# Performance work log

Measured on AMD Instinct MI355X. Metric: run time of the kernel, lower is better.

Reference implementation:

```python
import jax, jax.numpy as jnp
import numpy as np

EPS = 1e-5  # BatchNorm1d default eps


def gcn_conv(x, row, col, w, n):
    # symmetric normalized aggregation: out[c] = sum_e d[row]^-1/2 d[col]^-1/2 w_e x[row]
    deg = jax.ops.segment_sum(w, col, num_segments=n)           # weighted in-degree [N]
    dinv = jnp.where(deg > 0, jax.lax.rsqrt(deg), 0.0)          # nan_to_num guard
    norm = dinv[row] * dinv[col] * w                            # [E]
    msg = x[row] * norm[:, None]                                # [E, H] gather
    return jax.ops.segment_sum(msg, col, num_segments=n)        # [N, H] scatter-add


def batchnorm(x):
    # BatchNorm1d(affine=False, track_running_stats=False): batch stats, biased var
    mu = jnp.mean(x, axis=0)
    var = jnp.mean((x - mu) ** 2, axis=0)
    return (x - mu) * jax.lax.rsqrt(var + EPS)


def setup_inputs() -> dict:
    key = jax.random.key(0)
    ks = jax.random.split(key, 7)
    N, E, D, H = 100000, 1600000, 128, 128
    x = jax.random.normal(ks[0], (N, D), dtype=jnp.float32)
    edge_index = jax.random.randint(ks[1], (2, E), 0, N, dtype=jnp.int32)
    edge_weight = jax.random.uniform(ks[2], (E,), dtype=jnp.float32)
    # xavier_uniform gain=1: limit = sqrt(6/(fan_in+fan_out))
    lim0 = float(np.sqrt(6.0 / (D + H)))
    lim1 = float(np.sqrt(6.0 / (H + H)))
    W0 = jax.random.uniform(ks[3], (H, D), dtype=jnp.float32, minval=-lim0, maxval=lim0)
    W1 = jax.random.uniform(ks[4], (H, H), dtype=jnp.float32, minval=-lim1, maxval=lim1)
    b0 = jnp.zeros((H,), jnp.float32)
    b1 = jnp.zeros((H,), jnp.float32)
    return {"x": x, "edge_index": edge_index, "edge_weight": edge_weight,
            "W0": W0, "b0": b0, "W1": W1, "b1": b1}


def reference(x, edge_index, edge_weight, W0, b0, W1, b1):
    n = x.shape[0]
    row, col = edge_index[0], edge_index[1]
    # layer 0: linear -> gcn_conv -> bias -> batchnorm -> relu
    h = x @ W0.T
    h = gcn_conv(h, row, col, edge_weight, n)
    h = jax.nn.relu(batchnorm(h + b0))
    # final layer: linear -> gcn_conv -> bias
    h = h @ W1.T
    h = gcn_conv(h, row, col, edge_weight, n)
    return h + b1
```

## Files before the change

### kernel.cpp

```cpp
#include <hip/hip_runtime.h>
#include <cstdint>
#include <cstddef>

#define EPSF 1e-5f
#define BKT 256
#define BKT_SHIFT 8
#define SC_E 4096

typedef unsigned long long ull;
typedef __attribute__((ext_vector_type(8))) short bf16x8;
typedef __attribute__((ext_vector_type(4))) float f32x4;


__global__ __launch_bounds__(512) void bucket_hist(const int* __restrict__ col,
                                                   int* __restrict__ bhist, int E, int NB) {
    __shared__ int lh[512];
    const int t = threadIdx.x;
    lh[t] = 0;
    __syncthreads();
    for (int e = blockIdx.x * 512 + t; e < E; e += gridDim.x * 512)
        atomicAdd(&lh[col[e] >> BKT_SHIFT], 1);
    __syncthreads();
    if (t < NB && lh[t]) atomicAdd(&bhist[t], lh[t]);
}

__global__ __launch_bounds__(512) void scan_buckets(const int* __restrict__ bhist,
                                                    int* __restrict__ bstart,
                                                    int* __restrict__ bcursor,
                                                    int* __restrict__ rs,
                                                    int NB, int N, int E) {
    __shared__ int part[512];
    const int t = threadIdx.x;
    part[t] = (t < NB) ? bhist[t] : 0;
    __syncthreads();
    for (int off = 1; off < 512; off <<= 1) {
        int v = (t >= off) ? part[t - off] : 0;
        __syncthreads();
        part[t] += v;
        __syncthreads();
    }
    int excl = (t == 0) ? 0 : part[t - 1];
    if (t < NB) { bstart[t] = excl; bcursor[t] = excl; }
    if (t == 0) { bstart[NB] = E; rs[N] = E; }
}

__global__ __launch_bounds__(512) void bucket_scatter(const int* __restrict__ row,
                                                      const int* __restrict__ col,
                                                      const float* __restrict__ w,
                                                      int* __restrict__ bcursor,
                                                      int2* __restrict__ brecs,
                                                      int E, int NB) {
    __shared__ int lh[512], lstart[512], lcur[512], gbase[512];
    __shared__ int   sm[SC_E];
    __shared__ float sw[SC_E];
    __shared__ short sb[SC_E];

    const int t = threadIdx.x;
    const int base = blockIdx.x * SC_E;
    const int cnt = min(SC_E, E - base);

    lh[t] = 0;
    __syncthreads();

    int   myb[8], mym[8];
    float myw[8];
#pragma unroll
    for (int k = 0; k < 8; ++k) {
        int i = t + k * 512;
        if (i < cnt) {
            int e = base + i;
            int r = row[e], c = col[e];
            myb[k] = c >> BKT_SHIFT;
            mym[k] = ((c & (BKT - 1)) << 17) | r;
            myw[k] = w[e];
            atomicAdd(&lh[myb[k]], 1);
        } else myb[k] = -1;
    }
    __syncthreads();

    int v = lh[t];
    lstart[t] = v;
    __syncthreads();
    for (int off = 1; off < 512; off <<= 1) {
        int u = (t >= off) ? lstart[t - off] : 0;
        __syncthreads();
        lstart[t] += u;
        __syncthreads();
    }
    int excl = lstart[t] - v;
    __syncthreads();
    lstart[t] = excl;
    lcur[t]   = excl;
    gbase[t]  = (t < NB) ? atomicAdd(&bcursor[t], v) : 0;
    __syncthreads();

#pragma unroll
    for (int k = 0; k < 8; ++k) {
        if (myb[k] >= 0) {
            int slot = atomicAdd(&lcur[myb[k]], 1);
            sm[slot] = mym[k];
            sw[slot] = myw[k];
            sb[slot] = (short)myb[k];
        }
    }
    __syncthreads();

    for (int j = t; j < cnt; j += 512) {
        int b = sb[j];
        int pos = gbase[b] + (j - lstart[b]);
        brecs[pos] = make_int2(sm[j], __float_as_int(sw[j]));
    }
}

__global__ __launch_bounds__(256) void bucket_build(const int2* __restrict__ brecs,
                                                    const int* __restrict__ bstart,
                                                    int* __restrict__ rs,
                                                    float* __restrict__ dinv,
                                                    int2* __restrict__ sedge, int N) {
    __shared__ int   lcnt[256], lscan[256], lcur[256];
    __shared__ float ldeg[256];
    const int b = blockIdx.x, t = threadIdx.x;
    const int s = bstart[b], e = bstart[b + 1];
    const int node0 = b << BKT_SHIFT;
    const int nNodes = min(BKT, N - node0);

    lcnt[t] = 0;
    ldeg[t] = 0.f;
    __syncthreads();

    for (int i = s + t; i < e; i += 256) {
        int2 r = brecs[i];
        int cl = r.x >> 17;
        atomicAdd(&lcnt[cl], 1);
        atomicAdd(&ldeg[cl], __int_as_float(r.y));
    }
    __syncthreads();

    int v = lcnt[t];
    lscan[t] = v;
    __syncthreads();
    for (int off = 1; off < 256; off <<= 1) {
        int u = (t >= off) ? lscan[t - off] : 0;
        __syncthreads();
        lscan[t] += u;
        __syncthreads();
    }
    int excl = lscan[t] - v;
    lcur[t] = excl;
    if (t < nNodes) {
        rs[node0 + t] = s + excl;
        float d = ldeg[t];
        dinv[node0 + t] = (d > 0.f) ? rsqrtf(d) : 0.f;
    }
    __syncthreads();

    for (int i = s + t; i < e; i += 256) {
        int2 r = brecs[i];
        int slot = atomicAdd(&lcur[r.x >> 17], 1);
        sedge[s + slot] = r;
    }
}

__global__ __launch_bounds__(256) void norm_fixup(const int* __restrict__ bstart,
                                                  const float* __restrict__ dinv,
                                                  int2* __restrict__ sedge, int N) {
    __shared__ float ld[256];
    const int b = blockIdx.x, t = threadIdx.x;
    const int node0 = b << BKT_SHIFT;
    const int nNodes = min(BKT, N - node0);
    ld[t] = (t < nNodes) ? dinv[node0 + t] : 0.f;
    const int s = bstart[b], e = bstart[b + 1];
    __syncthreads();
    for (int i = s + t; i < e; i += 256) {
        int2 r = sedge[i];
        int rowi = r.x & 0x1FFFF;
        int cl = r.x >> 17;
        float nrm = dinv[rowi] * ld[cl] * __int_as_float(r.y);
        sedge[i] = make_int2(rowi, __float_as_int(nrm));
    }
}

__device__ __forceinline__ ushort f2bf(float f) {
    uint b = __float_as_uint(f);
    return (ushort)((b + 0x7FFFu + ((b >> 16) & 1u)) >> 16);
}
__device__ __forceinline__ float bf2f(ushort u) {
    return __uint_as_float((uint)u << 16);
}
__device__ __forceinline__ uint4 pack8(const float* f) {
    uint4 o;
    o.x = f2bf(f[0]) | ((uint)f2bf(f[1]) << 16);
    o.y = f2bf(f[2]) | ((uint)f2bf(f[3]) << 16);
    o.z = f2bf(f[4]) | ((uint)f2bf(f[5]) << 16);
    o.w = f2bf(f[6]) | ((uint)f2bf(f[7]) << 16);
    return o;
}

template <int MODE>
__global__ __launch_bounds__(256) void gemm128_mfma(const void* __restrict__ Xv,
                                                    const float* __restrict__ W,
                                                    ushort* __restrict__ Y, int N,
                                                    const float* __restrict__ sums,
                                                    float invN) {
    __shared__ __align__(16) ushort Alds[64][128];
    __shared__ __align__(16) ushort Blds[128][128];
    __shared__ float bnmu[128], bnrs[128];

    const int t  = threadIdx.x;
    const int n0 = blockIdx.x * 64;

    if constexpr (MODE == 2) {
        if (t < 128) {
            float mu  = sums[t] * invN;
            float var = sums[128 + t] * invN - mu * mu;
            bnmu[t] = mu;
            bnrs[t] = rsqrtf(var + EPSF);
        }
        __syncthreads();
    }

    for (int i = t; i < 128 * 16; i += 256) {
        int j = i >> 4, kc = (i & 15) << 3;
        float f[8];
        *(float4*)&f[0] = *(const float4*)&W[j * 128 + kc];
        *(float4*)&f[4] = *(const float4*)&W[j * 128 + kc + 4];
        *(uint4*)&Blds[j][kc ^ ((j & 7) << 3)] = pack8(f);
    }
    for (int i = t; i < 64 * 16; i += 256) {
        int r = i >> 4, kc = (i & 15) << 3;
        int n = n0 + r;
        uint4 v = make_uint4(0u, 0u, 0u, 0u);
        if (n < N) {
            if constexpr (MODE == 0) {
                float f[8];
                *(float4*)&f[0] = *(const float4*)&((const float*)Xv)[(size_t)n * 128 + kc];
                *(float4*)&f[4] = *(const float4*)&((const float*)Xv)[(size_t)n * 128 + kc + 4];
                v = pack8(f);
            } else {
                uint4 raw = *(const uint4*)&((const ushort*)Xv)[(size_t)n * 128 + kc];
                const uint* rw = &raw.x;
                float f[8];
#pragma unroll
                for (int k = 0; k < 4; ++k) {
                    float lo = __uint_as_float(rw[k] << 16);
                    float hi = __uint_as_float(rw[k] & 0xFFFF0000u);
                    f[2 * k]     = fmaxf((lo - bnmu[kc + 2 * k])     * bnrs[kc + 2 * k],     0.f);
                    f[2 * k + 1] = fmaxf((hi - bnmu[kc + 2 * k + 1]) * bnrs[kc + 2 * k + 1], 0.f);
                }
                v = pack8(f);
            }
        }
        *(uint4*)&Alds[r][kc ^ ((r & 7) << 3)] = v;
    }
    __syncthreads();

    const int lane  = t & 63;
    const int wv    = t >> 6;
    const int arow  = wv * 16 + (lane & 15);
    const int klane = (lane >> 4) << 3;
    const int cq    = lane & 15;

    f32x4 acc[8] = {};

    for (int ks = 0; ks < 4; ++ks) {
        const int k0 = ks * 32 + klane;
        bf16x8 a = *(const bf16x8*)&Alds[arow][k0 ^ ((arow & 7) << 3)];
#pragma unroll
        for (int tl = 0; tl < 8; ++tl) {
            int colr = tl * 16 + cq;
            bf16x8 bb = *(const bf16x8*)&Blds[colr][k0 ^ ((colr & 7) << 3)];
            acc[tl] = __builtin_amdgcn_mfma_f32_16x16x32_bf16(a, bb, acc[tl], 0, 0, 0);
        }
    }

    const int r0 = n0 + wv * 16 + ((lane >> 4) << 2);
#pragma unroll
    for (int tl = 0; tl < 8; ++tl) {
#pragma unroll
        for (int reg = 0; reg < 4; ++reg) {
            int rr = r0 + reg;
            if (rr < N) Y[(size_t)rr * 128 + tl * 16 + cq] = f2bf(acc[tl][reg]);
        }
    }
}

__device__ __forceinline__ float bflo(uint v) { return __uint_as_float(v << 16); }
__device__ __forceinline__ float bfhi(uint v) { return __uint_as_float(v & 0xFFFF0000u); }

template <bool OUT_BF16>
__global__ __launch_bounds__(256) void agg_gather(const ushort* __restrict__ Hin,
                                                  const int2* __restrict__ sedge,
                                                  const int* __restrict__ rs,
                                                  const float* __restrict__ bias,
                                                  void* __restrict__ Hout, int N, int E) {
    int c = blockIdx.x * 4 + (threadIdx.x >> 6);
    if (c >= N) return;
    const int lane = threadIdx.x & 63;

    float2 acc;
    if (bias) { acc.x = bias[lane * 2]; acc.y = bias[lane * 2 + 1]; }
    else      { acc.x = 0.f; acc.y = 0.f; }

    const int e0 = rs[c];
    const int deg = rs[c + 1] - e0;

    for (int base = 0; base < deg; base += 64) {
        int m = min(64, deg - base);
        int idx = e0 + base + lane;
        int2 rec = sedge[idx < E ? idx : E - 1];

        int j = 0;
        for (; j + 3 < m; j += 4) {
            int   r0 = __shfl(rec.x, j),     r1 = __shfl(rec.x, j + 1);
            int   r2 = __shfl(rec.x, j + 2), r3 = __shfl(rec.x, j + 3);
            float w0 = __int_as_float(__shfl(rec.y, j));
            float w1 = __int_as_float(__shfl(rec.y, j + 1));
            float w2 = __int_as_float(__shfl(rec.y, j + 2));
            float w3 = __int_as_float(__shfl(rec.y, j + 3));
            uint v0 = *(const uint*)&Hin[(size_t)r0 * 128 + lane * 2];
            uint v1 = *(const uint*)&Hin[(size_t)r1 * 128 + lane * 2];
            uint v2 = *(const uint*)&Hin[(size_t)r2 * 128 + lane * 2];
            uint v3 = *(const uint*)&Hin[(size_t)r3 * 128 + lane * 2];
            acc.x = fmaf(w0, bflo(v0), acc.x); acc.y = fmaf(w0, bfhi(v0), acc.y);
            acc.x = fmaf(w1, bflo(v1), acc.x); acc.y = fmaf(w1, bfhi(v1), acc.y);
            acc.x = fmaf(w2, bflo(v2), acc.x); acc.y = fmaf(w2, bfhi(v2), acc.y);
            acc.x = fmaf(w3, bflo(v3), acc.x); acc.y = fmaf(w3, bfhi(v3), acc.y);
        }
        for (; j < m; ++j) {
            int   r0 = __shfl(rec.x, j);
            float w0 = __int_as_float(__shfl(rec.y, j));
            uint v0 = *(const uint*)&Hin[(size_t)r0 * 128 + lane * 2];
            acc.x = fmaf(w0, bflo(v0), acc.x); acc.y = fmaf(w0, bfhi(v0), acc.y);
        }
    }

    if constexpr (OUT_BF16) {
        ((uint*)Hout)[(size_t)c * 64 + lane] = f2bf(acc.x) | ((uint)f2bf(acc.y) << 16);
    } else {
        *(float2*)&((float*)Hout)[(size_t)c * 128 + lane * 2] = acc;
    }
}

__global__ __launch_bounds__(256) void bn_stats(const ushort* __restrict__ H,
                                                float* __restrict__ sums, int N) {
    int j = threadIdx.x & 127;
    float s = 0.f, s2 = 0.f;
    for (int n = blockIdx.x * 2 + (threadIdx.x >> 7); n < N; n += gridDim.x * 2) {
        float v = bf2f(H[(size_t)n * 128 + j]);
        s += v; s2 += v * v;
    }
    atomicAdd(&sums[j], s);
    atomicAdd(&sums[128 + j], s2);
}

extern "C" void kernel_launch(void* const* d_in, const int* in_sizes, int n_in,
                              void* d_out, int out_size, void* d_ws, size_t ws_size,
                              hipStream_t stream) {
    const float* x  = (const float*)d_in[0];
    const int*   ei = (const int*)d_in[1];
    const float* ew = (const float*)d_in[2];
    const float* W0 = (const float*)d_in[3];
    const float* W1 = (const float*)d_in[5];
    const float* b1 = (const float*)d_in[6];

    const int N = in_sizes[0] / 128;
    const int E = in_sizes[2];
    const int* row = ei;
    const int* col = ei + E;
    const int NB = (N + BKT - 1) >> BKT_SHIFT;

    uintptr_t base = (uintptr_t)d_ws;
    auto alloc = [&](size_t bytes) {
        uintptr_t p = base;
        base += (bytes + 255) & ~(size_t)255;
        return (void*)p;
    };
    float*  dinv   = (float*) alloc((size_t)N * 4);
    float*  sums   = (float*) alloc(256 * 4);
    int*    bhist  = (int*)   alloc((size_t)(NB + 1) * 4);
    int*    bstart = (int*)   alloc((size_t)(NB + 1) * 4);
    int*    bcursor= (int*)   alloc((size_t)NB * 4);
    int*    rs     = (int*)   alloc((size_t)(N + 1) * 4);
    int2*   sedge  = (int2*)  alloc((size_t)E * 8);
    ushort* hA     = (ushort*)alloc((size_t)N * 128 * 2);
    ushort* hB     = (ushort*)alloc((size_t)N * 128 * 2);
    int2*   brecs  = (int2*)hB;
    float*  out    = (float*) d_out;
    (void)ws_size; (void)n_in; (void)out_size;

    const float invN = 1.f / (float)N;

    hipMemsetAsync(bhist, 0, (size_t)(NB + 1) * 4, stream);
    hipMemsetAsync(sums, 0, 256 * 4, stream);

    bucket_hist<<<1024, 512, 0, stream>>>(col, bhist, E, NB);
    scan_buckets<<<1, 512, 0, stream>>>(bhist, bstart, bcursor, rs, NB, N, E);
    bucket_scatter<<<(E + SC_E - 1) / SC_E, 512, 0, stream>>>(row, col, ew, bcursor,
                                                              brecs, E, NB);
    bucket_build<<<NB, 256, 0, stream>>>(brecs, bstart, rs, dinv, sedge, N);
    norm_fixup<<<NB, 256, 0, stream>>>(bstart, dinv, sedge, N);

    gemm128_mfma<0><<<(N + 63) / 64, 256, 0, stream>>>(x, W0, hA, N, nullptr, 0.f);

    agg_gather<true><<<(N + 3) / 4, 256, 0, stream>>>(hA, sedge, rs, nullptr, hB, N, E);

    bn_stats<<<512, 256, 0, stream>>>(hB, sums, N);

    gemm128_mfma<2><<<(N + 63) / 64, 256, 0, stream>>>(hB, W1, hA, N, sums, invN);

    agg_gather<false><<<(N + 3) / 4, 256, 0, stream>>>(hA, sedge, rs, b1, out, N, E);
}
```

Before: 305.6 us.

## Fuse norm fixup into edge placement, persist GEMM tiles, widen gather to half-wave edges

Three changes land together. The bucket build is split so that degree/dinv is computed first, and the placement pass then writes final normalized edge records directly, which removes the separate sedge re-read and re-write pass. The GEMM becomes a persistent grid-stride kernel capped at 512 blocks, so the bf16 weight tile is packed once per block instead of once per 64-row tile. The aggregation gather now has each half-wave process a different edge with 8-byte loads and combines the halves with a shuffle, raising memory-level parallelism per wave at the cost of a final reduction.

```diff
diff --git a/kernel.cpp b/kernel.cpp
--- a/kernel.cpp
+++ b/kernel.cpp
@@ -112,12 +112,11 @@
     }
 }
 
-__global__ __launch_bounds__(256) void bucket_build(const int2* __restrict__ brecs,
-                                                    const int* __restrict__ bstart,
-                                                    int* __restrict__ rs,
-                                                    float* __restrict__ dinv,
-                                                    int2* __restrict__ sedge, int N) {
-    __shared__ int   lcnt[256], lscan[256], lcur[256];
+__global__ __launch_bounds__(256) void bucket_build_p1(const int2* __restrict__ brecs,
+                                                       const int* __restrict__ bstart,
+                                                       int* __restrict__ rs,
+                                                       float* __restrict__ dinv, int N) {
+    __shared__ int   lcnt[256], lscan[256];
     __shared__ float ldeg[256];
     const int b = blockIdx.x, t = threadIdx.x;
     const int s = bstart[b], e = bstart[b + 1];
@@ -145,38 +144,36 @@
         lscan[t] += u;
         __syncthreads();
     }
-    int excl = lscan[t] - v;
-    lcur[t] = excl;
     if (t < nNodes) {
-        rs[node0 + t] = s + excl;
+        rs[node0 + t] = s + (lscan[t] - v);
         float d = ldeg[t];
         dinv[node0 + t] = (d > 0.f) ? rsqrtf(d) : 0.f;
     }
+}
+
+__global__ __launch_bounds__(256) void bucket_place(const int2* __restrict__ brecs,
+                                                    const int* __restrict__ bstart,
+                                                    const int* __restrict__ rs,
+                                                    const float* __restrict__ dinv,
+                                                    int2* __restrict__ sedge, int N) {
+    __shared__ int   lcur[256];
+    __shared__ float ld[256];
+    const int b = blockIdx.x, t = threadIdx.x;
+    const int s = bstart[b], e = bstart[b + 1];
+    const int node0 = b << BKT_SHIFT;
+    const int nNodes = min(BKT, N - node0);
+
+    lcur[t] = (t < nNodes) ? rs[node0 + t] : 0;
+    ld[t]   = (t < nNodes) ? dinv[node0 + t] : 0.f;
     __syncthreads();
 
     for (int i = s + t; i < e; i += 256) {
         int2 r = brecs[i];
-        int slot = atomicAdd(&lcur[r.x >> 17], 1);
-        sedge[s + slot] = r;
-    }
-}
-
-__global__ __launch_bounds__(256) void norm_fixup(const int* __restrict__ bstart,
-                                                  const float* __restrict__ dinv,
-                                                  int2* __restrict__ sedge, int N) {
-    __shared__ float ld[256];
-    const int b = blockIdx.x, t = threadIdx.x;
-    const int node0 = b << BKT_SHIFT;
-    const int nNodes = min(BKT, N - node0);
-    ld[t] = (t < nNodes) ? dinv[node0 + t] : 0.f;
-    const int s = bstart[b], e = bstart[b + 1];
-    __syncthreads();
-    for (int i = s + t; i < e; i += 256) {
-        int2 r = sedge[i];
+        int cl   = r.x >> 17;
         int rowi = r.x & 0x1FFFF;
-        int cl = r.x >> 17;
         float nrm = dinv[rowi] * ld[cl] * __int_as_float(r.y);
-        sedge[i] = make_int2(rowi, __float_as_int(nrm));
+        int slot = atomicAdd(&lcur[cl], 1);
+        sedge[slot] = make_int2(rowi, __float_as_int(nrm));
     }
 }
 
@@ -206,8 +203,7 @@
     __shared__ __align__(16) ushort Blds[128][128];
     __shared__ float bnmu[128], bnrs[128];
 
-    const int t  = threadIdx.x;
-    const int n0 = blockIdx.x * 64;
+    const int t = threadIdx.x;
 
     if constexpr (MODE == 2) {
         if (t < 128) {
@@ -216,7 +212,6 @@
             bnmu[t] = mu;
             bnrs[t] = rsqrtf(var + EPSF);
         }
-        __syncthreads();
     }
 
     for (int i = t; i < 128 * 16; i += 256) {
@@ -226,60 +221,66 @@
         *(float4*)&f[4] = *(const float4*)&W[j * 128 + kc + 4];
         *(uint4*)&Blds[j][kc ^ ((j & 7) << 3)] = pack8(f);
     }
-    for (int i = t; i < 64 * 16; i += 256) {
-        int r = i >> 4, kc = (i & 15) << 3;
-        int n = n0 + r;
-        uint4 v = make_uint4(0u, 0u, 0u, 0u);
-        if (n < N) {
-            if constexpr (MODE == 0) {
-                float f[8];
-                *(float4*)&f[0] = *(const float4*)&((const float*)Xv)[(size_t)n * 128 + kc];
-                *(float4*)&f[4] = *(const float4*)&((const float*)Xv)[(size_t)n * 128 + kc + 4];
-                v = pack8(f);
-            } else {
-                uint4 raw = *(const uint4*)&((const ushort*)Xv)[(size_t)n * 128 + kc];
-                const uint* rw = &raw.x;
-                float f[8];
-#pragma unroll
-                for (int k = 0; k < 4; ++k) {
-                    float lo = __uint_as_float(rw[k] << 16);
-                    float hi = __uint_as_float(rw[k] & 0xFFFF0000u);
-                    f[2 * k]     = fmaxf((lo - bnmu[kc + 2 * k])     * bnrs[kc + 2 * k],     0.f);
-                    f[2 * k + 1] = fmaxf((hi - bnmu[kc + 2 * k + 1]) * bnrs[kc + 2 * k + 1], 0.f);
-                }
-                v = pack8(f);
-            }
-        }
-        *(uint4*)&Alds[r][kc ^ ((r & 7) << 3)] = v;
-    }
-    __syncthreads();
 
     const int lane  = t & 63;
     const int wv    = t >> 6;
     const int arow  = wv * 16 + (lane & 15);
     const int klane = (lane >> 4) << 3;
     const int cq    = lane & 15;
-
-    f32x4 acc[8] = {};
-
-    for (int ks = 0; ks < 4; ++ks) {
-        const int k0 = ks * 32 + klane;
-        bf16x8 a = *(const bf16x8*)&Alds[arow][k0 ^ ((arow & 7) << 3)];
+    const int nTiles = (N + 63) >> 6;
+
+    for (int tile = blockIdx.x; tile < nTiles; tile += gridDim.x) {
+        const int n0 = tile * 64;
+        __syncthreads();
+
+        for (int i = t; i < 64 * 16; i += 256) {
+            int r = i >> 4, kc = (i & 15) << 3;
+            int n = n0 + r;
+            uint4 v = make_uint4(0u, 0u, 0u, 0u);
+            if (n < N) {
+                if constexpr (MODE == 0) {
+                    float f[8];
+                    *(float4*)&f[0] = *(const float4*)&((const float*)Xv)[(size_t)n * 128 + kc];
+                    *(float4*)&f[4] = *(const float4*)&((const float*)Xv)[(size_t)n * 128 + kc + 4];
+                    v = pack8(f);
+                } else {
+                    uint4 raw = *(const uint4*)&((const ushort*)Xv)[(size_t)n * 128 + kc];
+                    const uint* rw = &raw.x;
+                    float f[8];
+#pragma unroll
+                    for (int k = 0; k < 4; ++k) {
+                        float lo = __uint_as_float(rw[k] << 16);
+                        float hi = __uint_as_float(rw[k] & 0xFFFF0000u);
+                        f[2 * k]     = fmaxf((lo - bnmu[kc + 2 * k])     * bnrs[kc + 2 * k],     0.f);
+                        f[2 * k + 1] = fmaxf((hi - bnmu[kc + 2 * k + 1]) * bnrs[kc + 2 * k + 1], 0.f);
+                    }
+                    v = pack8(f);
+                }
+            }
+            *(uint4*)&Alds[r][kc ^ ((r & 7) << 3)] = v;
+        }
+        __syncthreads();
+
+        f32x4 acc[8] = {};
+        for (int ks = 0; ks < 4; ++ks) {
+            const int k0 = ks * 32 + klane;
+            bf16x8 a = *(const bf16x8*)&Alds[arow][k0 ^ ((arow & 7) << 3)];
+#pragma unroll
+            for (int tl = 0; tl < 8; ++tl) {
+                int colr = tl * 16 + cq;
+                bf16x8 bb = *(const bf16x8*)&Blds[colr][k0 ^ ((colr & 7) << 3)];
+                acc[tl] = __builtin_amdgcn_mfma_f32_16x16x32_bf16(a, bb, acc[tl], 0, 0, 0);
+            }
+        }
+
+        const int r0 = n0 + wv * 16 + ((lane >> 4) << 2);
 #pragma unroll
         for (int tl = 0; tl < 8; ++tl) {
-            int colr = tl * 16 + cq;
-            bf16x8 bb = *(const bf16x8*)&Blds[colr][k0 ^ ((colr & 7) << 3)];
-            acc[tl] = __builtin_amdgcn_mfma_f32_16x16x32_bf16(a, bb, acc[tl], 0, 0, 0);
-        }
-    }
-
-    const int r0 = n0 + wv * 16 + ((lane >> 4) << 2);
-#pragma unroll
-    for (int tl = 0; tl < 8; ++tl) {
-#pragma unroll
-        for (int reg = 0; reg < 4; ++reg) {
-            int rr = r0 + reg;
-            if (rr < N) Y[(size_t)rr * 128 + tl * 16 + cq] = f2bf(acc[tl][reg]);
+#pragma unroll
+            for (int reg = 0; reg < 4; ++reg) {
+                int rr = r0 + reg;
+                if (rr < N) Y[(size_t)rr * 128 + tl * 16 + cq] = f2bf(acc[tl][reg]);
+            }
         }
     }
 }
@@ -296,10 +297,11 @@
     int c = blockIdx.x * 4 + (threadIdx.x >> 6);
     if (c >= N) return;
     const int lane = threadIdx.x & 63;
-
-    float2 acc;
-    if (bias) { acc.x = bias[lane * 2]; acc.y = bias[lane * 2 + 1]; }
-    else      { acc.x = 0.f; acc.y = 0.f; }
+    const int h  = lane >> 5;
+    const int lq = lane & 31;
+
+    float4 acc = make_float4(0.f, 0.f, 0.f, 0.f);
+    if (bias && h == 0) acc = *(const float4*)&bias[lq * 4];
 
     const int e0 = rs[c];
     const int deg = rs[c + 1] - e0;
@@ -310,34 +312,46 @@
         int2 rec = sedge[idx < E ? idx : E - 1];
 
         int j = 0;
-        for (; j + 3 < m; j += 4) {
-            int   r0 = __shfl(rec.x, j),     r1 = __shfl(rec.x, j + 1);
-            int   r2 = __shfl(rec.x, j + 2), r3 = __shfl(rec.x, j + 3);
-            float w0 = __int_as_float(__shfl(rec.y, j));
-            float w1 = __int_as_float(__shfl(rec.y, j + 1));
-            float w2 = __int_as_float(__shfl(rec.y, j + 2));
-            float w3 = __int_as_float(__shfl(rec.y, j + 3));
-            uint v0 = *(const uint*)&Hin[(size_t)r0 * 128 + lane * 2];
-            uint v1 = *(const uint*)&Hin[(size_t)r1 * 128 + lane * 2];
-            uint v2 = *(const uint*)&Hin[(size_t)r2 * 128 + lane * 2];
-            uint v3 = *(const uint*)&Hin[(size_t)r3 * 128 + lane * 2];
-            acc.x = fmaf(w0, bflo(v0), acc.x); acc.y = fmaf(w0, bfhi(v0), acc.y);
-            acc.x = fmaf(w1, bflo(v1), acc.x); acc.y = fmaf(w1, bfhi(v1), acc.y);
-            acc.x = fmaf(w2, bflo(v2), acc.x); acc.y = fmaf(w2, bfhi(v2), acc.y);
-            acc.x = fmaf(w3, bflo(v3), acc.x); acc.y = fmaf(w3, bfhi(v3), acc.y);
-        }
-        for (; j < m; ++j) {
-            int   r0 = __shfl(rec.x, j);
-            float w0 = __int_as_float(__shfl(rec.y, j));
-            uint v0 = *(const uint*)&Hin[(size_t)r0 * 128 + lane * 2];
-            acc.x = fmaf(w0, bflo(v0), acc.x); acc.y = fmaf(w0, bfhi(v0), acc.y);
-        }
-    }
-
-    if constexpr (OUT_BF16) {
-        ((uint*)Hout)[(size_t)c * 64 + lane] = f2bf(acc.x) | ((uint)f2bf(acc.y) << 16);
-    } else {
-        *(float2*)&((float*)Hout)[(size_t)c * 128 + lane * 2] = acc;
+#define PLOAD(p, rr, ww, vv)                                                    \
+        int   rr = __shfl(rec.x, j + 2 * (p) + h);                              \
+        float ww = __int_as_float(__shfl(rec.y, j + 2 * (p) + h));              \
+        uint2 vv = *(const uint2*)&Hin[(size_t)rr * 128 + lq * 4];
+#define PACC(ww, vv)                                                            \
+        acc.x = fmaf(ww, bflo(vv.x), acc.x); acc.y = fmaf(ww, bfhi(vv.x), acc.y);\
+        acc.z = fmaf(ww, bflo(vv.y), acc.z); acc.w = fmaf(ww, bfhi(vv.y), acc.w);
+
+        for (; j + 7 < m; j += 8) {
+            PLOAD(0, r0, w0, v0) PLOAD(1, r1, w1, v1)
+            PLOAD(2, r2, w2, v2) PLOAD(3, r3, w3, v3)
+            PACC(w0, v0) PACC(w1, v1) PACC(w2, v2) PACC(w3, v3)
+        }
+        for (; j < m; j += 2) {
+            int jj = j + h;
+            int sl = (jj < m) ? jj : j;
+            int   r0 = __shfl(rec.x, sl);
+            float w0 = __int_as_float(__shfl(rec.y, sl));
+            if (jj >= m) w0 = 0.f;
+            uint2 v0 = *(const uint2*)&Hin[(size_t)r0 * 128 + lq * 4];
+            PACC(w0, v0)
+        }
+#undef PLOAD
+#undef PACC
+    }
+
+    acc.x += __shfl_xor(acc.x, 32);
+    acc.y += __shfl_xor(acc.y, 32);
+    acc.z += __shfl_xor(acc.z, 32);
+    acc.w += __shfl_xor(acc.w, 32);
+
+    if (h == 0) {
+        if constexpr (OUT_BF16) {
+            uint2 o;
+            o.x = f2bf(acc.x) | ((uint)f2bf(acc.y) << 16);
+            o.y = f2bf(acc.z) | ((uint)f2bf(acc.w) << 16);
+            *(uint2*)&((uint*)Hout)[(size_t)c * 64 + lq * 2] = o;
+        } else {
+            *(float4*)&((float*)Hout)[(size_t)c * 128 + lq * 4] = acc;
+        }
     }
 }
 
@@ -397,16 +411,19 @@
     scan_buckets<<<1, 512, 0, stream>>>(bhist, bstart, bcursor, rs, NB, N, E);
     bucket_scatter<<<(E + SC_E - 1) / SC_E, 512, 0, stream>>>(row, col, ew, bcursor,
                                                               brecs, E, NB);
-    bucket_build<<<NB, 256, 0, stream>>>(brecs, bstart, rs, dinv, sedge, N);
-    norm_fixup<<<NB, 256, 0, stream>>>(bstart, dinv, sedge, N);
-
-    gemm128_mfma<0><<<(N + 63) / 64, 256, 0, stream>>>(x, W0, hA, N, nullptr, 0.f);
+    bucket_build_p1<<<NB, 256, 0, stream>>>(brecs, bstart, rs, dinv, N);
+    bucket_place<<<NB, 256, 0, stream>>>(brecs, bstart, rs, dinv, sedge, N);
+
+    const int nTiles = (N + 63) / 64;
+    const int gemmGrid = nTiles < 512 ? nTiles : 512;
+
+    gemm128_mfma<0><<<gemmGrid, 256, 0, stream>>>(x, W0, hA, N, nullptr, 0.f);
 
     agg_gather<true><<<(N + 3) / 4, 256, 0, stream>>>(hA, sedge, rs, nullptr, hB, N, E);
 
     bn_stats<<<512, 256, 0, stream>>>(hB, sums, N);
 
-    gemm128_mfma<2><<<(N + 63) / 64, 256, 0, stream>>>(hB, W1, hA, N, sums, invN);
+    gemm128_mfma<2><<<gemmGrid, 256, 0, stream>>>(hB, W1, hA, N, sums, invN);
 
     agg_gather<false><<<(N + 3) / 4, 256, 0, stream>>>(hA, sedge, rs, b1, out, N, E);
 }
```

New measurement: 293.6 us. 3.9% less time.
